# Kernel optimization log

Hardware: AMD Instinct MI355X
Metric: run time of the kernel (lower is better)

Reference implementation:

```python
import jax, jax.numpy as jnp
import numpy as np

T, IN, R, OUT = 262144, 32, 50, 32
SPECTRAL_RADIUS = 0.95


def setup_inputs() -> dict:
    key = jax.random.key(0)
    kx, kw, kd, ko = jax.random.split(key, 4)
    X = jax.random.normal(kx, (T, IN), dtype=jnp.float32)
    # W_in ~ U(-1, 1), real-valued then cast to complex (zero imag), per source
    W_in = jax.random.uniform(kw, (R, IN), dtype=jnp.float32, minval=-1.0, maxval=1.0)
    # diagonal of W_res ~ U(-rho, rho)
    w_res_diag = jax.random.uniform(kd, (R,), dtype=jnp.float32, minval=-SPECTRAL_RADIUS, maxval=SPECTRAL_RADIUS)
    # dense1: Linear(R, OUT, bias=False) weight [OUT, R]
    W_out = jax.random.normal(ko, (OUT, R), dtype=jnp.float32) / np.sqrt(R).astype(np.float32)
    return {"X": X, "W_in": W_in, "w_res_diag": w_res_diag, "W_out": W_out}


def reference(X, W_in, w_res_diag, W_out):
    # fit(X): FFT -> sequential reservoir update -> dense -> IFFT
    Xc = jnp.fft.fft(X.astype(jnp.complex64), axis=0)            # [T, IN] complex64
    Wc = W_in.astype(jnp.complex64)                               # zero-imag params, as in source
    d = w_res_diag.astype(jnp.complex64)
    Woc = W_out.astype(jnp.complex64)

    proj = Xc @ Wc.T                                              # [T, R] input projections (parallel part)

    def step(state, p):
        # state_{t} = tanh(W_in @ x_t + diag(d) @ state_{t-1})
        s = jnp.tanh(p + d * state)
        return s, s

    s0 = jnp.zeros((R,), dtype=jnp.complex64)
    _, states = jax.lax.scan(step, s0, proj)                      # [T, R]

    out = states @ Woc.T                                          # [T, OUT]
    return jnp.fft.ifft(out, axis=0)                              # [T, OUT] complex64
```

## Files before the change

### kernel.cpp

```cpp
#include <hip/hip_runtime.h>
#include <hip/hip_fp16.h>
#include <math.h>


constexpr int TLEN = 262144;
constexpr int NCOL = 32;
constexpr int NR = 50;
constexpr int SCH = 64;
constexpr int LW = 28;
constexpr int ROWS = SCH + LW;
constexpr int CPB = 2;
constexpr int LDSTR = 51;
constexpr float TWO_PI = 6.28318530717958647692f;

__device__ __forceinline__ unsigned rev9(unsigned x) { return __brev(x) >> 23; }

template <int SIGN>
__device__ __forceinline__ void fft512(float2 (*lds)[9], int tid) {
  const int cl = tid & 7;
  const int bb = tid >> 3;
#pragma unroll
  for (int S = 0; S < 4; ++S) {
    const int h = 1 << (2 * S);
    const float inv4h = 1.0f / (float)(4 * h);
#pragma unroll
    for (int i = 0; i < 4; ++i) {
      const int q = bb + (i << 5);
      const int j = q & (h - 1);
      const int G = q >> (2 * S);
      const int i0 = (G << (2 * S + 2)) + j;
      float2 a0 = lds[i0][cl];
      float2 a1 = lds[i0 + h][cl];
      float2 a2 = lds[i0 + 2 * h][cl];
      float2 a3 = lds[i0 + 3 * h][cl];
      const float angp = (float)SIGN * TWO_PI * ((float)j * inv4h);
      float swp, cwp;
      __sincosf(angp, &swp, &cwp);
      const float cw = cwp * cwp - swp * swp;
      const float sw = 2.0f * cwp * swp;
      float2 t1 = make_float2(a1.x * cw - a1.y * sw, a1.x * sw + a1.y * cw);
      float2 t3 = make_float2(a3.x * cw - a3.y * sw, a3.x * sw + a3.y * cw);
      float2 u0 = make_float2(a0.x + t1.x, a0.y + t1.y);
      float2 u1 = make_float2(a0.x - t1.x, a0.y - t1.y);
      float2 u2 = make_float2(a2.x + t3.x, a2.y + t3.y);
      float2 u3 = make_float2(a2.x - t3.x, a2.y - t3.y);
      float2 r2 = make_float2(u2.x * cwp - u2.y * swp, u2.x * swp + u2.y * cwp);
      float2 r3 = make_float2(u3.x * cwp - u3.y * swp, u3.x * swp + u3.y * cwp);
      const float2 s3 = (SIGN < 0) ? make_float2(r3.y, -r3.x)
                                   : make_float2(-r3.y, r3.x);
      lds[i0][cl]         = make_float2(u0.x + r2.x, u0.y + r2.y);
      lds[i0 + 2 * h][cl] = make_float2(u0.x - r2.x, u0.y - r2.y);
      lds[i0 + h][cl]     = make_float2(u1.x + s3.x, u1.y + s3.y);
      lds[i0 + 3 * h][cl] = make_float2(u1.x - s3.x, u1.y - s3.y);
    }
    __syncthreads();
  }
  {
#pragma unroll
    for (int i = 0; i < 8; ++i) {
      const int j = bb + (i << 5);
      float2 a = lds[j][cl];
      float2 c = lds[j + 256][cl];
      const float ang = (float)SIGN * TWO_PI * ((float)j * (1.0f / 512.0f));
      float sw, cw;
      __sincosf(ang, &sw, &cw);
      float2 t = make_float2(c.x * cw - c.y * sw, c.x * sw + c.y * cw);
      lds[j][cl]       = make_float2(a.x + t.x, a.y + t.y);
      lds[j + 256][cl] = make_float2(a.x - t.x, a.y - t.y);
    }
    __syncthreads();
  }
}

template <int SIGN, int INMODE>
__global__ __launch_bounds__(256) void fft_passA(const void* __restrict__ vin,
                                                 float2* __restrict__ out,
                                                 float scale) {
  __shared__ float2 lds[512][9];
  const int nL = blockIdx.x;
  const int cg = blockIdx.y;
  const int tid = threadIdx.x;
  const int cl = tid & 7;
  const int cglob = cg * 8 + cl;
#pragma unroll
  for (int i = 0; i < 16; ++i) {
    const int nH = (tid >> 3) + (i << 5);
    const size_t gidx = (size_t)(nL + (nH << 9)) * NCOL + cglob;
    float2 v;
    if (INMODE == 0) {
      v = make_float2(((const float*)vin)[gidx], 0.0f);
    } else {
      const float2 f = __half22float2(((const __half2*)vin)[gidx]);
      v = make_float2(f.x * scale, f.y * scale);
    }
    lds[rev9(nH)][cl] = v;
  }
  __syncthreads();
  fft512<SIGN>(lds, tid);
#pragma unroll
  for (int i = 0; i < 16; ++i) {
    const int kL = (tid >> 3) + (i << 5);
    float2 v = lds[kL][cl];
    const float rev = (float)(nL * kL) * (1.0f / 262144.0f);
    const float ang = (float)SIGN * TWO_PI * rev;
    float sw, cw;
    __sincosf(ang, &sw, &cw);
    float2 w = make_float2(v.x * cw - v.y * sw, v.x * sw + v.y * cw);
    out[(size_t)(kL * 512 + nL) * NCOL + cglob] = w;
  }
}

template <int SIGN, bool REALOUT>
__global__ __launch_bounds__(256) void fft_passB(float2* __restrict__ buf,
                                                 float* __restrict__ rout) {
  __shared__ float2 lds[512][9];
  const int kL = blockIdx.x;
  const int cg = blockIdx.y;
  const int tid = threadIdx.x;
  const int cl = tid & 7;
  const int cglob = cg * 8 + cl;
#pragma unroll
  for (int i = 0; i < 16; ++i) {
    const int nL = (tid >> 3) + (i << 5);
    lds[rev9(nL)][cl] = buf[(size_t)(kL * 512 + nL) * NCOL + cglob];
  }
  __syncthreads();
  fft512<SIGN>(lds, tid);
#pragma unroll
  for (int i = 0; i < 16; ++i) {
    const int kH = (tid >> 3) + (i << 5);
    if (REALOUT) {
      rout[(size_t)(kL + (kH << 9)) * NCOL + cglob] = lds[kH][cl].x;
    } else {
      buf[(size_t)(kL * 512 + kH) * NCOL + cglob] = lds[kH][cl];
    }
  }
}

__device__ __forceinline__ void esn_step(float d, float pr, float pi,
                                         float& sr, float& si) {
  const float x = fmaf(d, sr, pr);
  const float y = fmaf(d, si, pi);
  float x2 = 2.0f * x;
  x2 = fminf(fmaxf(x2, -30.0f), 30.0f);
  const float E = __expf(x2);
  const float Ei = __expf(-x2);
  const float sh = 0.5f * (E - Ei);
  const float ch = 0.5f * (E + Ei);
  float s2, c2;
  __sincosf(2.0f * y, &s2, &c2);
  const float inv = __builtin_amdgcn_rcpf(ch + c2);
  sr = sh * inv;
  si = s2 * inv;
}

__global__ __launch_bounds__(256) void esn_scan_fused(
    const float2* __restrict__ Xc, const float* __restrict__ Win,
    const float* __restrict__ dvec, const float* __restrict__ Wout,
    __half2* __restrict__ outh) {
  __shared__ float2 buf[CPB][ROWS * LDSTR];
  const int tid = threadIdx.x;
  const int lane = tid & 63;
  const int wv = tid >> 6;
  const int cbase = blockIdx.x * CPB;

  {
    const int g = tid >> 7;
    const int row = tid & 127;
    if (row < ROWS) {
      const int t = (cbase + g) * SCH - LW + row;
      float2* dst = &buf[g][row * LDSTR];
      if (t < 0) {
        for (int r = 0; r < NR; ++r) dst[r] = make_float2(0.f, 0.f);
      } else {
        const size_t xrow = (size_t)(((t & 511) << 9) | (t >> 9));
        const float4* src = (const float4*)(Xc + xrow * NCOL);
        float2 xc[NCOL];
#pragma unroll
        for (int i = 0; i < NCOL / 2; ++i) {
          float4 v = src[i];
          xc[2 * i] = make_float2(v.x, v.y);
          xc[2 * i + 1] = make_float2(v.z, v.w);
        }
        for (int r = 0; r < NR; ++r) {
          float pr = 0.f, pi = 0.f;
#pragma unroll
          for (int c = 0; c < NCOL; ++c) {
            const float w = Win[r * NCOL + c];
            pr = fmaf(w, xc[c].x, pr);
            pi = fmaf(w, xc[c].y, pi);
          }
          dst[r] = make_float2(pr, pi);
        }
      }
    }
  }
  __syncthreads();

  if (lane < 25) {
    const int idx = wv * 25 + lane;
    const int c = idx / NR;
    const int r = idx - c * NR;
    const float d = dvec[r];
    float2* col = &buf[c][r];
    float sr = 0.f, si = 0.f;
    float2 p0 = col[0 * LDSTR];
    float2 p1 = col[1 * LDSTR];
    float2 p2 = col[2 * LDSTR];
    for (int i = 0; i < ROWS; ++i) {
      const float2 p = p0;
      p0 = p1;
      p1 = p2;
      const int ip = (i + 3 < ROWS) ? (i + 3) : (ROWS - 1);
      p2 = col[ip * LDSTR];
      esn_step(d, p.x, p.y, sr, si);
      if (i >= LW) col[i * LDSTR] = make_float2(sr, si);
    }
  }
  __syncthreads();

  const int wvu = __builtin_amdgcn_readfirstlane(wv);
#pragma unroll
  for (int p = 0; p < 2; ++p) {
    const int o0 = (wvu + (p << 2)) << 2;
    for (int c = 0; c < CPB; ++c) {
      const float2* srow = &buf[c][(LW + lane) * LDSTR];
      float ar0 = 0.f, ar1 = 0.f, ar2 = 0.f, ar3 = 0.f;
      float ai0 = 0.f, ai1 = 0.f, ai2 = 0.f, ai3 = 0.f;
      for (int r = 0; r < NR; ++r) {
        const float2 s = srow[r];
        const float w0 = Wout[(o0 + 0) * NR + r];
        const float w1 = Wout[(o0 + 1) * NR + r];
        const float w2 = Wout[(o0 + 2) * NR + r];
        const float w3 = Wout[(o0 + 3) * NR + r];
        ar0 = fmaf(w0, s.x, ar0); ai0 = fmaf(w0, s.y, ai0);
        ar1 = fmaf(w1, s.x, ar1); ai1 = fmaf(w1, s.y, ai1);
        ar2 = fmaf(w2, s.x, ar2); ai2 = fmaf(w2, s.y, ai2);
        ar3 = fmaf(w3, s.x, ar3); ai3 = fmaf(w3, s.y, ai3);
      }
      __half2* orow = &outh[((size_t)(cbase + c) * SCH + lane) * NCOL + o0];
      orow[0] = __floats2half2_rn(ar0, ai0);
      orow[1] = __floats2half2_rn(ar1, ai1);
      orow[2] = __floats2half2_rn(ar2, ai2);
      orow[3] = __floats2half2_rn(ar3, ai3);
    }
  }
}

extern "C" void kernel_launch(void* const* d_in, const int* in_sizes, int n_in,
                              void* d_out, int out_size, void* d_ws, size_t ws_size,
                              hipStream_t stream) {
  const float* X = (const float*)d_in[0];
  const float* Win = (const float*)d_in[1];
  const float* dvec = (const float*)d_in[2];
  const float* Wout = (const float*)d_in[3];

  float2* Wa = (float2*)d_ws;
  dim3 fgrid(512, 4);

  fft_passA<-1, 0><<<fgrid, 256, 0, stream>>>(X, Wa, 1.0f);
  fft_passB<-1, false><<<fgrid, 256, 0, stream>>>(Wa, nullptr);
  esn_scan_fused<<<TLEN / SCH / CPB, 256, 0, stream>>>(Wa, Win, dvec, Wout,
                                                       (__half2*)d_out);
  fft_passA<1, 1><<<fgrid, 256, 0, stream>>>(d_out, Wa, 1.0f / 262144.0f);
  fft_passB<1, true><<<fgrid, 256, 0, stream>>>(Wa, (float*)d_out);

  (void)in_sizes; (void)n_in; (void)out_size; (void)ws_size;
}
```

Baseline: 343.0 us.

## Pack real FFT column pairs into complex transforms to halve FFT work

The forward FFT now treats pairs of real input columns as one complex signal, which halves the number of FFT columns and the grid. The consumer separates the two spectra using the conjugate-symmetric index (T-t). The inverse FFT packs two complex output columns into one transform whose real and imaginary parts give the two outputs, and writes them as float2. This is meant to halve FFT arithmetic and memory traffic, at the cost of extra mirrored-row gathers and combine arithmetic in the scan kernel and the inverse pass A.

```diff
diff --git a/kernel.cpp b/kernel.cpp
--- a/kernel.cpp
+++ b/kernel.cpp
@@ -5,6 +5,7 @@
 
 constexpr int TLEN = 262144;
 constexpr int NCOL = 32;
+constexpr int NCOLP = 16;
 constexpr int NR = 50;
 constexpr int SCH = 64;
 constexpr int LW = 28;
@@ -85,13 +86,19 @@
 #pragma unroll
   for (int i = 0; i < 16; ++i) {
     const int nH = (tid >> 3) + (i << 5);
-    const size_t gidx = (size_t)(nL + (nH << 9)) * NCOL + cglob;
+    const size_t k = (size_t)(nL + (nH << 9));
     float2 v;
     if (INMODE == 0) {
-      v = make_float2(((const float*)vin)[gidx], 0.0f);
+      v = ((const float2*)vin)[k * NCOLP + cglob];
     } else {
-      const float2 f = __half22float2(((const __half2*)vin)[gidx]);
-      v = make_float2(f.x * scale, f.y * scale);
+      const size_t m = (TLEN - k) & (TLEN - 1);
+      const __half2* hin = (const __half2*)vin;
+      const float2 va = __half22float2(hin[k * NCOL + 2 * cglob]);
+      const float2 vb = __half22float2(hin[k * NCOL + 2 * cglob + 1]);
+      const float2 wa = __half22float2(hin[m * NCOL + 2 * cglob]);
+      const float2 wb = __half22float2(hin[m * NCOL + 2 * cglob + 1]);
+      v = make_float2(scale * (va.x + wa.x - vb.y + wb.y),
+                      scale * (va.y - wa.y + vb.x + wb.x));
     }
     lds[rev9(nH)][cl] = v;
   }
@@ -106,7 +113,7 @@
     float sw, cw;
     __sincosf(ang, &sw, &cw);
     float2 w = make_float2(v.x * cw - v.y * sw, v.x * sw + v.y * cw);
-    out[(size_t)(kL * 512 + nL) * NCOL + cglob] = w;
+    out[(size_t)(kL * 512 + nL) * NCOLP + cglob] = w;
   }
 }
 
@@ -122,7 +129,7 @@
 #pragma unroll
   for (int i = 0; i < 16; ++i) {
     const int nL = (tid >> 3) + (i << 5);
-    lds[rev9(nL)][cl] = buf[(size_t)(kL * 512 + nL) * NCOL + cglob];
+    lds[rev9(nL)][cl] = buf[(size_t)(kL * 512 + nL) * NCOLP + cglob];
   }
   __syncthreads();
   fft512<SIGN>(lds, tid);
@@ -130,9 +137,9 @@
   for (int i = 0; i < 16; ++i) {
     const int kH = (tid >> 3) + (i << 5);
     if (REALOUT) {
-      rout[(size_t)(kL + (kH << 9)) * NCOL + cglob] = lds[kH][cl].x;
+      ((float2*)rout)[(size_t)(kL + (kH << 9)) * NCOLP + cglob] = lds[kH][cl];
     } else {
-      buf[(size_t)(kL * 512 + kH) * NCOL + cglob] = lds[kH][cl];
+      buf[(size_t)(kL * 512 + kH) * NCOLP + cglob] = lds[kH][cl];
     }
   }
 }
@@ -174,13 +181,22 @@
         for (int r = 0; r < NR; ++r) dst[r] = make_float2(0.f, 0.f);
       } else {
         const size_t xrow = (size_t)(((t & 511) << 9) | (t >> 9));
-        const float4* src = (const float4*)(Xc + xrow * NCOL);
+        const int tm = (TLEN - t) & (TLEN - 1);
+        const size_t xrowm = (size_t)(((tm & 511) << 9) | (tm >> 9));
+        const float4* src = (const float4*)(Xc + xrow * NCOLP);
+        const float4* srcm = (const float4*)(Xc + xrowm * NCOLP);
+        float4 z4[8], m4[8];
+#pragma unroll
+        for (int i = 0; i < 8; ++i) { z4[i] = src[i]; m4[i] = srcm[i]; }
         float2 xc[NCOL];
 #pragma unroll
-        for (int i = 0; i < NCOL / 2; ++i) {
-          float4 v = src[i];
-          xc[2 * i] = make_float2(v.x, v.y);
-          xc[2 * i + 1] = make_float2(v.z, v.w);
+        for (int c = 0; c < NCOLP; ++c) {
+          const float zx = (c & 1) ? z4[c >> 1].z : z4[c >> 1].x;
+          const float zy = (c & 1) ? z4[c >> 1].w : z4[c >> 1].y;
+          const float mx = (c & 1) ? m4[c >> 1].z : m4[c >> 1].x;
+          const float my = (c & 1) ? m4[c >> 1].w : m4[c >> 1].y;
+          xc[2 * c]     = make_float2(0.5f * (zx + mx), 0.5f * (zy - my));
+          xc[2 * c + 1] = make_float2(0.5f * (zy + my), 0.5f * (mx - zx));
         }
         for (int r = 0; r < NR; ++r) {
           float pr = 0.f, pi = 0.f;
@@ -256,13 +272,13 @@
   const float* Wout = (const float*)d_in[3];
 
   float2* Wa = (float2*)d_ws;
-  dim3 fgrid(512, 4);
+  dim3 fgrid(512, 2);
 
   fft_passA<-1, 0><<<fgrid, 256, 0, stream>>>(X, Wa, 1.0f);
   fft_passB<-1, false><<<fgrid, 256, 0, stream>>>(Wa, nullptr);
   esn_scan_fused<<<TLEN / SCH / CPB, 256, 0, stream>>>(Wa, Win, dvec, Wout,
                                                        (__half2*)d_out);
-  fft_passA<1, 1><<<fgrid, 256, 0, stream>>>(d_out, Wa, 1.0f / 262144.0f);
+  fft_passA<1, 1><<<fgrid, 256, 0, stream>>>(d_out, Wa, 0.5f / 262144.0f);
   fft_passB<1, true><<<fgrid, 256, 0, stream>>>(Wa, (float*)d_out);
 
   (void)in_sizes; (void)n_in; (void)out_size; (void)ws_size;
```

Measured after the change: 286.1 us. -16.6%, faster.
